# Optimization experiments

Hardware: AMD Instinct MI355X
Metric: run time of the kernel (lower is better)

Reference implementation:

```python
import jax, jax.numpy as jnp
import numpy as np

HID = 64      # HIDDEN_DIM
VOCAB = 64    # VOCAB_SIZE
INNER = 24    # INNER_DIM
SEQ = 32      # SEQ_LEN
CAP = 8       # CAPACITY_LIMIT (deque maxlen)
LR = 0.05     # INFERENCE_LR
B1, B2, EPS = 0.9, 0.999, 1e-8   # torch Adam defaults
LN_EPS = 1e-5                    # torch LayerNorm default
BATCH = 8192


def setup_inputs() -> dict:
    key = jax.random.key(0)
    ks = jax.random.split(key, 8)
    def w(k, shape, s=0.02):
        return jax.random.normal(k, shape, jnp.float32) * s
    return {
        "seqs": jax.random.randint(ks[0], (BATCH, SEQ), 0, VOCAB, dtype=jnp.int32),
        "embed": w(ks[1], (VOCAB, HID), 1.0),
        "ff_w1": w(ks[2], (HID, 2 * HID)), "ff_b1": jnp.zeros((2 * HID,), jnp.float32),
        "ff_w2": w(ks[3], (2 * HID, HID)), "ff_b2": jnp.zeros((HID,), jnp.float32),
        "ln_g": jnp.ones((HID,), jnp.float32), "ln_b": jnp.zeros((HID,), jnp.float32),
        "mlp_w1": w(ks[4], (HID, INNER), 0.1), "mlp_b1": jnp.zeros((INNER,), jnp.float32),
        "mlp_w2": w(ks[5], (INNER, HID), 0.1), "mlp_b2": jnp.zeros((HID,), jnp.float32),
        "out_w": w(ks[6], (HID, VOCAB)), "out_b": jnp.zeros((VOCAB,), jnp.float32),
    }


def _mlp(p, x):
    w1, b1, w2, b2 = p
    return jnp.maximum(x @ w1 + b1, 0.0) @ w2 + b2


def reference(seqs, embed, ff_w1, ff_b1, ff_w2, ff_b2, ln_g, ln_b,
              mlp_w1, mlp_b1, mlp_w2, mlp_b2, out_w, out_b):
    # Encoder over all tokens used (t = 0..SEQ-2), batched: [B, 31, HID]
    h = embed[seqs[:, : SEQ - 1]]
    f = jnp.maximum(h @ ff_w1 + ff_b1, 0.0) @ ff_w2 + ff_b2
    x = h + f
    mu = x.mean(-1, keepdims=True)
    var = ((x - mu) ** 2).mean(-1, keepdims=True)
    enc = ln_g * (x - mu) * jax.lax.rsqrt(var + LN_EPS) + ln_b

    # deque(maxlen=8) over pairs (t even -> key, t odd -> val) keeps last 8 pairs:
    # keys at t = 14,16,...,28 ; vals at t = 15,17,...,29. Entries are detached.
    keys = jax.lax.stop_gradient(enc[:, 14:29:2])  # [B, 8, HID]
    vals = jax.lax.stop_gradient(enc[:, 15:30:2])  # [B, 8, HID]
    q = enc[:, SEQ - 2]                            # [B, HID]

    # load_state_dict copy breaks the graph -> base MLP params are constants here
    p0 = tuple(jax.lax.stop_gradient(p) for p in (mlp_w1, mlp_b1, mlp_w2, mlp_b2))
    steps = jnp.arange(1, CAP + 1, dtype=jnp.float32)

    def per_sample(k_i, v_i, q_i):
        def adam_step(carry, kv):
            p, m, v = carry
            kh, vh, t = kv
            g = jax.grad(lambda pp: jnp.mean((_mlp(pp, kh) - vh) ** 2))(p)
            m = jax.tree_util.tree_map(lambda a, b: B1 * a + (1.0 - B1) * b, m, g)
            v = jax.tree_util.tree_map(lambda a, b: B2 * a + (1.0 - B2) * b * b, v, g)
            bc1 = 1.0 - B1 ** t
            bc2 = 1.0 - B2 ** t
            p = jax.tree_util.tree_map(
                lambda pp, mm, vv: pp - LR * (mm / bc1) / (jnp.sqrt(vv / bc2) + EPS),
                p, m, v)
            return (p, m, v), None
        zeros = jax.tree_util.tree_map(jnp.zeros_like, p0)
        (pT, _, _), _ = jax.lax.scan(adam_step, (p0, zeros, zeros), (k_i, v_i, steps))
        return _mlp(pT, q_i)

    hq = jax.vmap(per_sample)(keys, vals, q)   # [B, HID]
    return hq @ out_w + out_b                  # [B, VOCAB]
```

## Files before the change

kernel.cpp:

```cpp
#include <hip/hip_runtime.h>
#include <hip/hip_bf16.h>
#include <math.h>

#define HID   64
#define VOCABN 64
#define INNER 24
#define SEQN  32
#define CAPN  8
#define NPOS  17
#define BATCHN 8192

typedef float f32x4 __attribute__((ext_vector_type(4)));
typedef float f32x2 __attribute__((ext_vector_type(2)));

#if defined(__has_builtin)
#  if __has_builtin(__builtin_elementwise_fma)
#    define PK_FMA(a,b,c) __builtin_elementwise_fma((a),(b),(c))
#  endif
#  if __has_builtin(__builtin_elementwise_max)
#    define PK_MAX(a,b) __builtin_elementwise_max((a),(b))
#  endif
#endif
#ifndef PK_FMA
static __device__ __forceinline__ f32x2 pk_fma_fb(f32x2 a, f32x2 b, f32x2 c) {
  f32x2 r; r.x = fmaf(a.x, b.x, c.x); r.y = fmaf(a.y, b.y, c.y); return r;
}
#  define PK_FMA(a,b,c) pk_fma_fb((a),(b),(c))
#endif
#ifndef PK_MAX
static __device__ __forceinline__ f32x2 pk_max_fb(f32x2 a, f32x2 b) {
  f32x2 r; r.x = fmaxf(a.x, b.x); r.y = fmaxf(a.y, b.y); return r;
}
#  define PK_MAX(a,b) pk_max_fb((a),(b))
#endif

static __device__ __forceinline__ f32x2 sp2(float x) { return (f32x2){x, x}; }

static __device__ const float CMSBR[8] = {
  0.01581139f, 0.01176584f, 0.01010053f, 0.00918844f,
  0.00862495f, 0.00825540f, 0.00800653f, 0.00783856f
};

__device__ __forceinline__ float allred32(float x) {
  int y;
  y = __builtin_amdgcn_update_dpp(__float_as_int(x), __float_as_int(x),
                                  0xB1, 0xF, 0xF, false);
  x += __int_as_float(y);
  y = __builtin_amdgcn_update_dpp(__float_as_int(x), __float_as_int(x),
                                  0x4E, 0xF, 0xF, false);
  x += __int_as_float(y);
  x += __int_as_float(__builtin_amdgcn_ds_swizzle(__float_as_int(x), 0x101F));
  x += __int_as_float(__builtin_amdgcn_ds_swizzle(__float_as_int(x), 0x201F));
  x += __int_as_float(__builtin_amdgcn_ds_swizzle(__float_as_int(x), 0x401F));
  return x;
}

__global__ __launch_bounds__(128) void build_table(
    const float* __restrict__ embed,
    const float* __restrict__ ff_w1,
    const float* __restrict__ ff_b1,
    const float* __restrict__ ff_w2,
    const float* __restrict__ ff_b2,
    const float* __restrict__ ln_g,
    const float* __restrict__ ln_b,
    float* __restrict__ etab)
{
  __shared__ float h[64];
  __shared__ float A1[128];
  __shared__ float xs[64];
  const int r = blockIdx.x;
  const int t = threadIdx.x;

  if (t < 64) h[t] = embed[r * 64 + t];
  __syncthreads();

  {
    float acc = ff_b1[t];
    #pragma unroll 8
    for (int k = 0; k < 64; ++k)
      acc = fmaf(h[k], ff_w1[k * 128 + t], acc);
    A1[t] = fmaxf(acc, 0.f);
  }
  __syncthreads();

  if (t < 64) {
    float acc = ff_b2[t];
    #pragma unroll 8
    for (int k = 0; k < 128; ++k)
      acc = fmaf(A1[k], ff_w2[k * 64 + t], acc);
    xs[t] = acc + h[t];
  }
  __syncthreads();

  if (t < 64) {
    float s1 = 0.f;
    if (t < 4)
      for (int j = 0; j < 16; ++j) s1 += xs[t + 4 * j];
    s1 += __shfl_xor(s1, 1);
    s1 += __shfl_xor(s1, 2);
    s1 = __shfl(s1, 0);
    float mu = s1 * 0.015625f;

    float s2 = 0.f;
    if (t < 4)
      for (int j = 0; j < 16; ++j) {
        float d = xs[t + 4 * j] - mu;
        s2 = fmaf(d, d, s2);
      }
    s2 += __shfl_xor(s2, 1);
    s2 += __shfl_xor(s2, 2);
    s2 = __shfl(s2, 0);
    float var = s2 * 0.015625f;
    float rs  = rsqrtf(var + 1e-5f);

    etab[r * 64 + t] = fmaf((xs[t] - mu) * rs, ln_g[t], ln_b[t]);
  }
}

__device__ __forceinline__ void adam_pk(f32x2& p, f32x2& m, f32x2& v,
                                        f32x2 g1, f32x2 g2, float cmsbr) {
  m = PK_FMA(sp2(0.9f),   m, g1);
  v = PK_FMA(sp2(0.999f), v, g2);
  f32x2 vc = PK_MAX(v, sp2(1e-30f));
  f32x2 r; r.x = __builtin_amdgcn_rsqf(vc.x); r.y = __builtin_amdgcn_rsqf(vc.y);
  f32x2 t = m * sp2(cmsbr);
  p = PK_FMA(-t, r, p);
}

__global__ __launch_bounds__(128, 3) void adapt_kernel(
    const int* __restrict__ seqs,
    const float* __restrict__ etab,
    const float* __restrict__ mlp_w1,
    const float* __restrict__ mlp_b1,
    const float* __restrict__ mlp_w2,
    const float* __restrict__ mlp_b2,
    const float* __restrict__ out_w,
    const float* __restrict__ out_b,
    float* __restrict__ out)
{
  __shared__ f32x2 yb[2][2][2][32];
  __shared__ __align__(16) float hqv[64];
  const int t    = threadIdx.x;
  const int lane = t & 63;
  const int w    = t >> 6;
  const int h    = lane >> 5;
  const int u    = lane & 31;
  const int s    = blockIdx.x;
  const int off  = 12 * w + 6 * h;

  const int* __restrict__ srow = seqs + s * SEQN + 14;

  f32x2 w1[6], m1[6], v1[6], w2[6], m2[6], v2[6];
  #pragma unroll
  for (int m = 0; m < 6; ++m) {
    f32x2 a; a.x = mlp_w1[(2 * u) * INNER + off + m];
             a.y = mlp_w1[(2 * u + 1) * INNER + off + m];
    w1[m] = a;
    w2[m] = *(const f32x2*)&mlp_w2[(off + m) * HID + 2 * u];
    m1[m] = sp2(0.f); v1[m] = sp2(0.f); m2[m] = sp2(0.f); v2[m] = sp2(0.f);
  }
  const int  d    = u - 3 * h;
  const bool own1 = ((unsigned)d < 3u);
  f32x2 b1v = own1 ? *(const f32x2*)&mlp_b1[off + 2 * d] : sp2(0.f);
  f32x2 mb1 = sp2(0.f), vb1 = sp2(0.f);
  const bool w0h0 = (w == 0) && (h == 0);
  f32x2 b2v = w0h0 ? *(const f32x2*)&mlp_b2[2 * u] : sp2(0.f);
  f32x2 mb2 = sp2(0.f), vb2 = sp2(0.f);

  const bool o0 = (u == 3 * h);
  const bool o1 = (u == 3 * h + 1);
  const bool o2 = (u == 3 * h + 2);

  const f32x2* e2 = (const f32x2*)etab;
  f32x2 kp = e2[srow[0] * 32 + u];
  f32x2 vp = e2[srow[1] * 32 + u];

  #pragma unroll 1
  for (int st = 0; st < 8; ++st) {
    const float cmsbr = CMSBR[st];

    f32x2 pz[6];
    #pragma unroll
    for (int m = 0; m < 6; ++m) pz[m] = kp * w1[m];
    pz[0].x += o0 ? b1v.x : 0.f;  pz[1].y += o0 ? b1v.y : 0.f;
    pz[2].x += o1 ? b1v.x : 0.f;  pz[3].y += o1 ? b1v.y : 0.f;
    pz[4].x += o2 ? b1v.x : 0.f;  pz[5].y += o2 ? b1v.y : 0.f;
    float a_[6];
    #pragma unroll
    for (int m = 0; m < 6; ++m) a_[m] = allred32(pz[m].x + pz[m].y);
    #pragma unroll
    for (int m = 0; m < 6; ++m) a_[m] = fmaxf(a_[m], 0.f);

    f32x2 yp = w0h0 ? b2v : sp2(0.f);
    #pragma unroll
    for (int m = 0; m < 6; ++m) yp = PK_FMA(sp2(a_[m]), w2[m], yp);
    yb[st & 1][w][h][u] = yp;
    __syncthreads();
    f32x2 q00 = yb[st & 1][0][0][u];
    f32x2 q01 = yb[st & 1][0][1][u];
    f32x2 q10 = yb[st & 1][1][0][u];
    f32x2 q11 = yb[st & 1][1][1][u];
    f32x2 ys  = (q00 + q01) + (q10 + q11);
    f32x2 dyv = (ys - vp) * sp2(0.03125f);

    int pp1 = 2 * st + 2; pp1 = pp1 < 16 ? pp1 : 16;
    int pp2 = 2 * st + 3; pp2 = pp2 < 16 ? pp2 : 16;
    f32x2 kn = e2[srow[pp1] * 32 + u];
    f32x2 vn = e2[srow[pp2] * 32 + u];

    float dz[6];
    #pragma unroll
    for (int m = 0; m < 6; ++m) {
      f32x2 bb = w2[m] * dyv;
      dz[m] = allred32(bb.x + bb.y);
    }
    #pragma unroll
    for (int m = 0; m < 6; ++m) dz[m] = (a_[m] > 0.f) ? dz[m] : 0.f;

    f32x2 k01  = kp * sp2(0.1f);
    f32x2 ksq  = (sp2(0.001f) * kp) * kp;
    f32x2 dy01 = dyv * sp2(0.1f);
    f32x2 dysq = (sp2(0.001f) * dyv) * dyv;
    #pragma unroll
    for (int m = 0; m < 6; ++m) {
      float dzs = dz[m] * dz[m];
      adam_pk(w1[m], m1[m], v1[m], k01 * sp2(dz[m]), ksq * sp2(dzs), cmsbr);
      float as = a_[m] * a_[m];
      adam_pk(w2[m], m2[m], v2[m], dy01 * sp2(a_[m]), dysq * sp2(as), cmsbr);
    }
    float glo = o0 ? dz[0] : (o1 ? dz[2] : dz[4]);
    float ghi = o0 ? dz[1] : (o1 ? dz[3] : dz[5]);
    f32x2 g1b; g1b.x = 0.1f * glo;           g1b.y = 0.1f * ghi;
    f32x2 g2b; g2b.x = 0.001f * (glo * glo); g2b.y = 0.001f * (ghi * ghi);
    adam_pk(b1v, mb1, vb1, g1b, g2b, cmsbr);
    if (w == 0) adam_pk(b2v, mb2, vb2, dy01, dysq, cmsbr);

    kp = kn; vp = vn;
  }

  {
    f32x2 pz[6];
    #pragma unroll
    for (int m = 0; m < 6; ++m) pz[m] = kp * w1[m];
    pz[0].x += o0 ? b1v.x : 0.f;  pz[1].y += o0 ? b1v.y : 0.f;
    pz[2].x += o1 ? b1v.x : 0.f;  pz[3].y += o1 ? b1v.y : 0.f;
    pz[4].x += o2 ? b1v.x : 0.f;  pz[5].y += o2 ? b1v.y : 0.f;
    f32x2 hpv = w0h0 ? b2v : sp2(0.f);
    #pragma unroll
    for (int m = 0; m < 6; ++m) {
      float aq = fmaxf(allred32(pz[m].x + pz[m].y), 0.f);
      hpv = PK_FMA(sp2(aq), w2[m], hpv);
    }
    yb[0][w][h][u] = hpv;
  }
  __syncthreads();
  if (t < 32) {
    f32x2 f00 = yb[0][0][0][u], f01 = yb[0][0][1][u];
    f32x2 f10 = yb[0][1][0][u], f11 = yb[0][1][1][u];
    *(f32x2*)&hqv[2 * u] = (f00 + f01) + (f10 + f11);
  }
  __syncthreads();

  if (w == 0) {
    float acc = out_b[lane];
    const f32x4* hv = (const f32x4*)hqv;
    #pragma unroll
    for (int j4 = 0; j4 < 16; ++j4) {
      f32x4 h4 = hv[j4];
      acc = fmaf(h4.x, out_w[(4 * j4 + 0) * 64 + lane], acc);
      acc = fmaf(h4.y, out_w[(4 * j4 + 1) * 64 + lane], acc);
      acc = fmaf(h4.z, out_w[(4 * j4 + 2) * 64 + lane], acc);
      acc = fmaf(h4.w, out_w[(4 * j4 + 3) * 64 + lane], acc);
    }
    out[(size_t)s * 64 + lane] = acc;
  }
}

extern "C" void kernel_launch(void* const* d_in, const int* in_sizes, int n_in,
                              void* d_out, int out_size, void* d_ws, size_t ws_size,
                              hipStream_t stream) {
  const int*   seqs   = (const int*)d_in[0];
  const float* embed  = (const float*)d_in[1];
  const float* ff_w1  = (const float*)d_in[2];
  const float* ff_b1  = (const float*)d_in[3];
  const float* ff_w2  = (const float*)d_in[4];
  const float* ff_b2  = (const float*)d_in[5];
  const float* ln_g   = (const float*)d_in[6];
  const float* ln_b   = (const float*)d_in[7];
  const float* mlp_w1 = (const float*)d_in[8];
  const float* mlp_b1 = (const float*)d_in[9];
  const float* mlp_w2 = (const float*)d_in[10];
  const float* mlp_b2 = (const float*)d_in[11];
  const float* out_w  = (const float*)d_in[12];
  const float* out_b  = (const float*)d_in[13];

  float* etab = (float*)d_ws;

  build_table<<<64, 128, 0, stream>>>(
      embed, ff_w1, ff_b1, ff_w2, ff_b2, ln_g, ln_b, etab);
  adapt_kernel<<<BATCHN, 128, 0, stream>>>(
      seqs, etab, mlp_w1, mlp_b1, mlp_w2, mlp_b2, out_w, out_b,
      (float*)d_out);
}
```

Baseline: 179.6 us.

## Map one sample per wavefront, removing block-level syncs in Adam loop

```diff
diff --git a/kernel.cpp b/kernel.cpp
--- a/kernel.cpp
+++ b/kernel.cpp
@@ -13,27 +13,12 @@
 typedef float f32x4 __attribute__((ext_vector_type(4)));
 typedef float f32x2 __attribute__((ext_vector_type(2)));
 
-#if defined(__has_builtin)
-#  if __has_builtin(__builtin_elementwise_fma)
-#    define PK_FMA(a,b,c) __builtin_elementwise_fma((a),(b),(c))
-#  endif
-#  if __has_builtin(__builtin_elementwise_max)
-#    define PK_MAX(a,b) __builtin_elementwise_max((a),(b))
-#  endif
-#endif
-#ifndef PK_FMA
-static __device__ __forceinline__ f32x2 pk_fma_fb(f32x2 a, f32x2 b, f32x2 c) {
+static __device__ __forceinline__ f32x2 pk_fma2(f32x2 a, f32x2 b, f32x2 c) {
   f32x2 r; r.x = fmaf(a.x, b.x, c.x); r.y = fmaf(a.y, b.y, c.y); return r;
 }
-#  define PK_FMA(a,b,c) pk_fma_fb((a),(b),(c))
-#endif
-#ifndef PK_MAX
-static __device__ __forceinline__ f32x2 pk_max_fb(f32x2 a, f32x2 b) {
+static __device__ __forceinline__ f32x2 pk_max2(f32x2 a, f32x2 b) {
   f32x2 r; r.x = fmaxf(a.x, b.x); r.y = fmaxf(a.y, b.y); return r;
 }
-#  define PK_MAX(a,b) pk_max_fb((a),(b))
-#endif
-
 static __device__ __forceinline__ f32x2 sp2(float x) { return (f32x2){x, x}; }
 
 static __device__ const float CMSBR[8] = {
@@ -119,15 +104,15 @@
 
 __device__ __forceinline__ void adam_pk(f32x2& p, f32x2& m, f32x2& v,
                                         f32x2 g1, f32x2 g2, float cmsbr) {
-  m = PK_FMA(sp2(0.9f),   m, g1);
-  v = PK_FMA(sp2(0.999f), v, g2);
-  f32x2 vc = PK_MAX(v, sp2(1e-30f));
+  m = pk_fma2(sp2(0.9f),   m, g1);
+  v = pk_fma2(sp2(0.999f), v, g2);
+  f32x2 vc = pk_max2(v, sp2(1e-30f));
   f32x2 r; r.x = __builtin_amdgcn_rsqf(vc.x); r.y = __builtin_amdgcn_rsqf(vc.y);
   f32x2 t = m * sp2(cmsbr);
-  p = PK_FMA(-t, r, p);
-}
-
-__global__ __launch_bounds__(128, 3) void adapt_kernel(
+  p = pk_fma2(-t, r, p);
+}
+
+__global__ __launch_bounds__(256, 2) void adapt_kernel(
     const int* __restrict__ seqs,
     const float* __restrict__ etab,
     const float* __restrict__ mlp_w1,
@@ -138,38 +123,34 @@
     const float* __restrict__ out_b,
     float* __restrict__ out)
 {
-  __shared__ f32x2 yb[2][2][2][32];
-  __shared__ __align__(16) float hqv[64];
+  __shared__ __align__(16) float hqv[4][64];
   const int t    = threadIdx.x;
+  const int wv   = t >> 6;
   const int lane = t & 63;
-  const int w    = t >> 6;
   const int h    = lane >> 5;
   const int u    = lane & 31;
-  const int s    = blockIdx.x;
-  const int off  = 12 * w + 6 * h;
+  const int s    = blockIdx.x * 4 + wv;
+  const int off  = 12 * h;
 
   const int* __restrict__ srow = seqs + s * SEQN + 14;
 
-  f32x2 w1[6], m1[6], v1[6], w2[6], m2[6], v2[6];
+  f32x2 w1[12], m1[12], v1[12], w2[12], m2[12], v2[12];
   #pragma unroll
-  for (int m = 0; m < 6; ++m) {
+  for (int m = 0; m < 12; ++m) {
     f32x2 a; a.x = mlp_w1[(2 * u) * INNER + off + m];
              a.y = mlp_w1[(2 * u + 1) * INNER + off + m];
     w1[m] = a;
     w2[m] = *(const f32x2*)&mlp_w2[(off + m) * HID + 2 * u];
     m1[m] = sp2(0.f); v1[m] = sp2(0.f); m2[m] = sp2(0.f); v2[m] = sp2(0.f);
   }
-  const int  d    = u - 3 * h;
-  const bool own1 = ((unsigned)d < 3u);
-  f32x2 b1v = own1 ? *(const f32x2*)&mlp_b1[off + 2 * d] : sp2(0.f);
+  const bool own1 = (u < 6);
+  f32x2 b1v = own1 ? *(const f32x2*)&mlp_b1[off + 2 * u] : sp2(0.f);
   f32x2 mb1 = sp2(0.f), vb1 = sp2(0.f);
-  const bool w0h0 = (w == 0) && (h == 0);
-  f32x2 b2v = w0h0 ? *(const f32x2*)&mlp_b2[2 * u] : sp2(0.f);
+  f32x2 b2v = (h == 0) ? *(const f32x2*)&mlp_b2[2 * u] : sp2(0.f);
   f32x2 mb2 = sp2(0.f), vb2 = sp2(0.f);
 
-  const bool o0 = (u == 3 * h);
-  const bool o1 = (u == 3 * h + 1);
-  const bool o2 = (u == 3 * h + 2);
+  const bool ou0 = (u == 0), ou1 = (u == 1), ou2 = (u == 2);
+  const bool ou3 = (u == 3), ou4 = (u == 4), ou5 = (u == 5);
 
   const f32x2* e2 = (const f32x2*)etab;
   f32x2 kp = e2[srow[0] * 32 + u];
@@ -179,28 +160,30 @@
   for (int st = 0; st < 8; ++st) {
     const float cmsbr = CMSBR[st];
 
-    f32x2 pz[6];
-    #pragma unroll
-    for (int m = 0; m < 6; ++m) pz[m] = kp * w1[m];
-    pz[0].x += o0 ? b1v.x : 0.f;  pz[1].y += o0 ? b1v.y : 0.f;
-    pz[2].x += o1 ? b1v.x : 0.f;  pz[3].y += o1 ? b1v.y : 0.f;
-    pz[4].x += o2 ? b1v.x : 0.f;  pz[5].y += o2 ? b1v.y : 0.f;
-    float a_[6];
-    #pragma unroll
-    for (int m = 0; m < 6; ++m) a_[m] = allred32(pz[m].x + pz[m].y);
-    #pragma unroll
-    for (int m = 0; m < 6; ++m) a_[m] = fmaxf(a_[m], 0.f);
-
-    f32x2 yp = w0h0 ? b2v : sp2(0.f);
-    #pragma unroll
-    for (int m = 0; m < 6; ++m) yp = PK_FMA(sp2(a_[m]), w2[m], yp);
-    yb[st & 1][w][h][u] = yp;
-    __syncthreads();
-    f32x2 q00 = yb[st & 1][0][0][u];
-    f32x2 q01 = yb[st & 1][0][1][u];
-    f32x2 q10 = yb[st & 1][1][0][u];
-    f32x2 q11 = yb[st & 1][1][1][u];
-    f32x2 ys  = (q00 + q01) + (q10 + q11);
+    f32x2 pz[12];
+    #pragma unroll
+    for (int m = 0; m < 12; ++m) pz[m] = kp * w1[m];
+    pz[0].x  += ou0 ? b1v.x : 0.f;  pz[1].y  += ou0 ? b1v.y : 0.f;
+    pz[2].x  += ou1 ? b1v.x : 0.f;  pz[3].y  += ou1 ? b1v.y : 0.f;
+    pz[4].x  += ou2 ? b1v.x : 0.f;  pz[5].y  += ou2 ? b1v.y : 0.f;
+    pz[6].x  += ou3 ? b1v.x : 0.f;  pz[7].y  += ou3 ? b1v.y : 0.f;
+    pz[8].x  += ou4 ? b1v.x : 0.f;  pz[9].y  += ou4 ? b1v.y : 0.f;
+    pz[10].x += ou5 ? b1v.x : 0.f;  pz[11].y += ou5 ? b1v.y : 0.f;
+    float a_[12];
+    #pragma unroll
+    for (int m = 0; m < 12; ++m) a_[m] = allred32(pz[m].x + pz[m].y);
+    #pragma unroll
+    for (int m = 0; m < 12; ++m) a_[m] = fmaxf(a_[m], 0.f);
+
+    f32x2 qA = (h == 0) ? b2v : sp2(0.f);
+    #pragma unroll
+    for (int m = 0; m < 6; ++m)  qA = pk_fma2(sp2(a_[m]), w2[m], qA);
+    f32x2 qB = sp2(0.f);
+    #pragma unroll
+    for (int m = 6; m < 12; ++m) qB = pk_fma2(sp2(a_[m]), w2[m], qB);
+    f32x2 sH = qA + qB;
+    f32x2 sO; sO.x = __shfl_xor(sH.x, 32); sO.y = __shfl_xor(sH.y, 32);
+    f32x2 ys  = sH + sO;
     f32x2 dyv = (ys - vp) * sp2(0.03125f);
 
     int pp1 = 2 * st + 2; pp1 = pp1 < 16 ? pp1 : 16;
@@ -208,62 +191,67 @@
     f32x2 kn = e2[srow[pp1] * 32 + u];
     f32x2 vn = e2[srow[pp2] * 32 + u];
 
-    float dz[6];
-    #pragma unroll
-    for (int m = 0; m < 6; ++m) {
+    float dz[12];
+    #pragma unroll
+    for (int m = 0; m < 12; ++m) {
       f32x2 bb = w2[m] * dyv;
       dz[m] = allred32(bb.x + bb.y);
     }
     #pragma unroll
-    for (int m = 0; m < 6; ++m) dz[m] = (a_[m] > 0.f) ? dz[m] : 0.f;
+    for (int m = 0; m < 12; ++m) dz[m] = (a_[m] > 0.f) ? dz[m] : 0.f;
 
     f32x2 k01  = kp * sp2(0.1f);
     f32x2 ksq  = (sp2(0.001f) * kp) * kp;
     f32x2 dy01 = dyv * sp2(0.1f);
     f32x2 dysq = (sp2(0.001f) * dyv) * dyv;
     #pragma unroll
-    for (int m = 0; m < 6; ++m) {
+    for (int m = 0; m < 12; ++m) {
       float dzs = dz[m] * dz[m];
       adam_pk(w1[m], m1[m], v1[m], k01 * sp2(dz[m]), ksq * sp2(dzs), cmsbr);
       float as = a_[m] * a_[m];
       adam_pk(w2[m], m2[m], v2[m], dy01 * sp2(a_[m]), dysq * sp2(as), cmsbr);
     }
-    float glo = o0 ? dz[0] : (o1 ? dz[2] : dz[4]);
-    float ghi = o0 ? dz[1] : (o1 ? dz[3] : dz[5]);
+    float glo = ou0 ? dz[0] : ou1 ? dz[2] : ou2 ? dz[4]
+              : ou3 ? dz[6] : ou4 ? dz[8] : dz[10];
+    float ghi = ou0 ? dz[1] : ou1 ? dz[3] : ou2 ? dz[5]
+              : ou3 ? dz[7] : ou4 ? dz[9] : dz[11];
     f32x2 g1b; g1b.x = 0.1f * glo;           g1b.y = 0.1f * ghi;
     f32x2 g2b; g2b.x = 0.001f * (glo * glo); g2b.y = 0.001f * (ghi * ghi);
     adam_pk(b1v, mb1, vb1, g1b, g2b, cmsbr);
-    if (w == 0) adam_pk(b2v, mb2, vb2, dy01, dysq, cmsbr);
+    adam_pk(b2v, mb2, vb2, dy01, dysq, cmsbr);
 
     kp = kn; vp = vn;
   }
 
   {
-    f32x2 pz[6];
-    #pragma unroll
-    for (int m = 0; m < 6; ++m) pz[m] = kp * w1[m];
-    pz[0].x += o0 ? b1v.x : 0.f;  pz[1].y += o0 ? b1v.y : 0.f;
-    pz[2].x += o1 ? b1v.x : 0.f;  pz[3].y += o1 ? b1v.y : 0.f;
-    pz[4].x += o2 ? b1v.x : 0.f;  pz[5].y += o2 ? b1v.y : 0.f;
-    f32x2 hpv = w0h0 ? b2v : sp2(0.f);
-    #pragma unroll
-    for (int m = 0; m < 6; ++m) {
-      float aq = fmaxf(allred32(pz[m].x + pz[m].y), 0.f);
-      hpv = PK_FMA(sp2(aq), w2[m], hpv);
-    }
-    yb[0][w][h][u] = hpv;
-  }
-  __syncthreads();
-  if (t < 32) {
-    f32x2 f00 = yb[0][0][0][u], f01 = yb[0][0][1][u];
-    f32x2 f10 = yb[0][1][0][u], f11 = yb[0][1][1][u];
-    *(f32x2*)&hqv[2 * u] = (f00 + f01) + (f10 + f11);
-  }
-  __syncthreads();
-
-  if (w == 0) {
+    f32x2 pz[12];
+    #pragma unroll
+    for (int m = 0; m < 12; ++m) pz[m] = kp * w1[m];
+    pz[0].x  += ou0 ? b1v.x : 0.f;  pz[1].y  += ou0 ? b1v.y : 0.f;
+    pz[2].x  += ou1 ? b1v.x : 0.f;  pz[3].y  += ou1 ? b1v.y : 0.f;
+    pz[4].x  += ou2 ? b1v.x : 0.f;  pz[5].y  += ou2 ? b1v.y : 0.f;
+    pz[6].x  += ou3 ? b1v.x : 0.f;  pz[7].y  += ou3 ? b1v.y : 0.f;
+    pz[8].x  += ou4 ? b1v.x : 0.f;  pz[9].y  += ou4 ? b1v.y : 0.f;
+    pz[10].x += ou5 ? b1v.x : 0.f;  pz[11].y += ou5 ? b1v.y : 0.f;
+    float aq[12];
+    #pragma unroll
+    for (int m = 0; m < 12; ++m) aq[m] = fmaxf(allred32(pz[m].x + pz[m].y), 0.f);
+    f32x2 qA = (h == 0) ? b2v : sp2(0.f);
+    #pragma unroll
+    for (int m = 0; m < 6; ++m)  qA = pk_fma2(sp2(aq[m]), w2[m], qA);
+    f32x2 qB = sp2(0.f);
+    #pragma unroll
+    for (int m = 6; m < 12; ++m) qB = pk_fma2(sp2(aq[m]), w2[m], qB);
+    f32x2 sH = qA + qB;
+    f32x2 sO; sO.x = __shfl_xor(sH.x, 32); sO.y = __shfl_xor(sH.y, 32);
+    f32x2 hq = sH + sO;
+    if (h == 0) *(f32x2*)&hqv[wv][2 * u] = hq;
+  }
+  __syncthreads();
+
+  {
     float acc = out_b[lane];
-    const f32x4* hv = (const f32x4*)hqv;
+    const f32x4* hv = (const f32x4*)hqv[wv];
     #pragma unroll
     for (int j4 = 0; j4 < 16; ++j4) {
       f32x4 h4 = hv[j4];
@@ -298,7 +286,7 @@
 
   build_table<<<64, 128, 0, stream>>>(
       embed, ff_w1, ff_b1, ff_w2, ff_b2, ln_g, ln_b, etab);
-  adapt_kernel<<<BATCHN, 128, 0, stream>>>(
+  adapt_kernel<<<BATCHN / 4, 256, 0, stream>>>(
       seqs, etab, mlp_w1, mlp_b1, mlp_w2, mlp_b2, out_w, out_b,
       (float*)d_out);
 }
```

After: 179.7 us. Within noise of the previous version (+0.1%).
